# Performance work log

Hardware: AMD Instinct MI355X
Metric: run time of the kernel (lower is better)

The kernel has to match this reference:

```python
import jax, jax.numpy as jnp
import numpy as np

B, S, D = 4, 4096, 1024


def setup_inputs() -> dict:
    key = jax.random.key(0)
    ks = jax.random.split(key, 4)
    scale = 1.0 / np.sqrt(D)
    x = jax.random.normal(ks[0], (B, S, D), dtype=jnp.float32)
    Wg = jax.random.normal(ks[1], (D, D), dtype=jnp.float32) * scale
    Wv = jax.random.normal(ks[2], (D, D), dtype=jnp.float32) * scale
    Wd = jax.random.normal(ks[3], (D, D), dtype=jnp.float32) * scale
    bg = jnp.zeros((D,), dtype=jnp.float32)
    bv = jnp.zeros((D,), dtype=jnp.float32)
    bd = jnp.ones((D,), dtype=jnp.float32)  # decay_bias_init = 1.0
    return {"x": x, "Wg": Wg, "bg": bg, "Wv": Wv, "bv": bv, "Wd": Wd, "bd": bd}


def _scan_causal(x_scan, a):
    # h_t = a_t * h_{t-1} + x_t, scanned over time; x_scan, a: [B,S,D]
    def step(h, inp):
        a_t, x_t = inp
        h = a_t * h + x_t
        return h, h

    h0 = jnp.zeros(x_scan.shape[::2], dtype=x_scan.dtype)  # [B,D]
    xs = (jnp.swapaxes(a, 0, 1), jnp.swapaxes(x_scan, 0, 1))  # [S,B,D]
    _, out = jax.lax.scan(step, h0, xs)
    return jnp.swapaxes(out, 0, 1)  # back to [B,S,D]


def reference(x, Wg, bg, Wv, bv, Wd, bd):
    # nn.Linear: y = x @ W.T + b
    g = jnp.einsum('bsd,ed->bse', x, Wg) + bg
    v = jnp.einsum('bsd,ed->bse', x, Wv) + bv
    d = jnp.einsum('bsd,ed->bse', x, Wd) + bd
    x_scan = jax.nn.sigmoid(g) * jnp.tanh(v)
    a = 0.001 + 0.998 * jax.nn.sigmoid(d)
    return _scan_causal(x_scan, a)
```

## Files before the change

### kernel.cpp

```cpp
#include <hip/hip_runtime.h>
#include <cstddef>
#include <cstdint>


typedef _Float16 f16;
typedef f16 f16x4 __attribute__((ext_vector_type(4)));
typedef f16 f16x8 __attribute__((ext_vector_type(8)));
typedef float f32x4 __attribute__((ext_vector_type(4)));

#define S_LEN 4096
#define D_DIM 1024
#define B_DIM 4
#define M_TOT (B_DIM * S_LEN)
#define N_TOT (3 * D_DIM)
#define K_TOT D_DIM

#define CHUNKS 128
#define CLEN (S_LEN / CHUNKS)

__global__ void cvt_f16_kernel(const float* __restrict__ src, f16* __restrict__ dst, int n) {
  int i = (blockIdx.x * blockDim.x + threadIdx.x) * 8;
  if (i >= n) return;
  f32x4 a = *(const f32x4*)(src + i);
  f32x4 b = *(const f32x4*)(src + i + 4);
  f16x8 o;
  o[0] = (f16)a[0]; o[1] = (f16)a[1]; o[2] = (f16)a[2]; o[3] = (f16)a[3];
  o[4] = (f16)b[0]; o[5] = (f16)b[1]; o[6] = (f16)b[2]; o[7] = (f16)b[3];
  *(f16x8*)(dst + i) = o;
}

#define BM 128
#define BN 128
#define BK 32

__device__ __forceinline__ void gl_lds16(const void* g, void* l) {
  __builtin_amdgcn_global_load_lds((const __attribute__((address_space(1))) void*)g,
                                   (__attribute__((address_space(3))) void*)l, 16, 0, 0);
}

__global__ __launch_bounds__(256) void gemm_f16_kernel(const f16* __restrict__ A,
                                                       const f16* __restrict__ Bt,
                                                       f16* __restrict__ C) {
  __shared__ __attribute__((aligned(16))) f16 As[BM * BK];
  __shared__ __attribute__((aligned(16))) f16 Bs[BN * BK];
  const int tid = threadIdx.x;
  const int lane = tid & 63;
  const int wave = tid >> 6;
  const int m0 = blockIdx.y * BM;
  const int n0 = blockIdx.x * BN;

  const int srow = tid >> 2;
  const int scol = (tid & 3) * 8;
  const f16* aG0 = A + (size_t)(m0 + srow) * K_TOT + scol;
  const f16* aG1 = A + (size_t)(m0 + srow + 64) * K_TOT + scol;
  const f16* bG0 = Bt + (size_t)(n0 + srow) * K_TOT + scol;
  const f16* bG1 = Bt + (size_t)(n0 + srow + 64) * K_TOT + scol;
  f16* aL0 = &As[tid * 8];
  f16* aL1 = &As[2048 + tid * 8];
  f16* bL0 = &Bs[tid * 8];
  f16* bL1 = &Bs[2048 + tid * 8];

  const int wm = (wave >> 1) * 64;
  const int wn = (wave & 1) * 64;
  const int lm = lane & 15;
  const int kq = (lane >> 4) * 8;

  f32x4 acc[4][4] = {};

  for (int k0 = 0; k0 < K_TOT; k0 += BK) {
    gl_lds16(aG0 + k0, aL0);
    gl_lds16(aG1 + k0, aL1);
    gl_lds16(bG0 + k0, bL0);
    gl_lds16(bG1 + k0, bL1);
    __syncthreads();
    f16x8 af[4], bf[4];
#pragma unroll
    for (int i = 0; i < 4; ++i)
      af[i] = *(const f16x8*)&As[(wm + i * 16 + lm) * BK + kq];
#pragma unroll
    for (int j = 0; j < 4; ++j)
      bf[j] = *(const f16x8*)&Bs[(wn + j * 16 + lm) * BK + kq];
#pragma unroll
    for (int i = 0; i < 4; ++i)
#pragma unroll
      for (int j = 0; j < 4; ++j)
        acc[i][j] = __builtin_amdgcn_mfma_f32_16x16x32_f16(af[i], bf[j], acc[i][j], 0, 0, 0);
    __syncthreads();
  }

  const int cm = m0 + wm + (lane >> 4) * 4;
  const int cn = n0 + wn + (lane & 15);
#pragma unroll
  for (int i = 0; i < 4; ++i)
#pragma unroll
    for (int j = 0; j < 4; ++j)
#pragma unroll
      for (int r = 0; r < 4; ++r)
        C[(size_t)(cm + i * 16 + r) * N_TOT + (cn + j * 16)] = (f16)acc[i][j][r];
}

__global__ void scan1_kernel(const f16* __restrict__ G, const float* __restrict__ bg,
                             const float* __restrict__ bv, const float* __restrict__ bd,
                             f16* __restrict__ xsA, f16* __restrict__ aA,
                             float* __restrict__ P, float* __restrict__ H) {
  const int u = blockIdx.x * 256 + threadIdx.x;
  const int cg = u & 255;
  const int b = (u >> 8) & 3;
  const int ck = u >> 10;
  const int ch = cg * 4;
  const f32x4 vbg = *(const f32x4*)(bg + ch);
  const f32x4 vbv = *(const f32x4*)(bv + ch);
  const f32x4 vbd = *(const f32x4*)(bd + ch);
  f32x4 h = {0.f, 0.f, 0.f, 0.f};
  f32x4 p = {1.f, 1.f, 1.f, 1.f};
  const int t0 = ck * CLEN;
#pragma unroll 4
  for (int t = t0; t < t0 + CLEN; ++t) {
    const size_t m = (size_t)b * S_LEN + t;
    const f16* gp = G + m * N_TOT + ch;
    f16x4 g4 = *(const f16x4*)gp;
    f16x4 v4 = *(const f16x4*)(gp + D_DIM);
    f16x4 d4 = *(const f16x4*)(gp + 2 * D_DIM);
    f16x4 xs4, a4;
#pragma unroll
    for (int j = 0; j < 4; ++j) {
      float gg = (float)g4[j] + vbg[j];
      float vv = (float)v4[j] + vbv[j];
      float dd = (float)d4[j] + vbd[j];
      float sg = 1.f / (1.f + __expf(-gg));
      float tv = 1.f - 2.f / (__expf(2.f * vv) + 1.f);
      float sd = 1.f / (1.f + __expf(-dd));
      f16 xh = (f16)(sg * tv);
      f16 ah = (f16)(0.001f + 0.998f * sd);
      float xsr = (float)xh, avr = (float)ah;
      h[j] = avr * h[j] + xsr;
      p[j] *= avr;
      xs4[j] = xh;
      a4[j] = ah;
    }
    *(f16x4*)(xsA + m * D_DIM + ch) = xs4;
    *(f16x4*)(aA + m * D_DIM + ch) = a4;
  }
  const int idx = ck * 4096 + b * D_DIM + ch;
  *(f32x4*)(P + idx) = p;
  *(f32x4*)(H + idx) = h;
}

__global__ void scan2_kernel(const float* __restrict__ P, const float* __restrict__ H,
                             float* __restrict__ carry) {
  const int idx = blockIdx.x * 256 + threadIdx.x;
  float h = 0.f;
  for (int c = 0; c < CHUNKS; ++c) {
    carry[c * 4096 + idx] = h;
    h = P[c * 4096 + idx] * h + H[c * 4096 + idx];
  }
}

__global__ void scan3_kernel(const f16* __restrict__ xsA, const f16* __restrict__ aA,
                             const float* __restrict__ carry, float* __restrict__ out) {
  const int u = blockIdx.x * 256 + threadIdx.x;
  const int cg = u & 255;
  const int b = (u >> 8) & 3;
  const int ck = u >> 10;
  const int ch = cg * 4;
  f32x4 h = *(const f32x4*)(carry + ck * 4096 + b * D_DIM + ch);
  const int t0 = ck * CLEN;
#pragma unroll 4
  for (int t = t0; t < t0 + CLEN; ++t) {
    const size_t m = (size_t)b * S_LEN + t;
    f16x4 xs4 = *(const f16x4*)(xsA + m * D_DIM + ch);
    f16x4 a4 = *(const f16x4*)(aA + m * D_DIM + ch);
#pragma unroll
    for (int j = 0; j < 4; ++j) h[j] = (float)a4[j] * h[j] + (float)xs4[j];
    *(f32x4*)(out + m * D_DIM + ch) = h;
  }
}

extern "C" void kernel_launch(void* const* d_in, const int* in_sizes, int n_in,
                              void* d_out, int out_size, void* d_ws, size_t ws_size,
                              hipStream_t stream) {
  const float* x = (const float*)d_in[0];
  const float* Wg = (const float*)d_in[1];
  const float* bg = (const float*)d_in[2];
  const float* Wv = (const float*)d_in[3];
  const float* bv = (const float*)d_in[4];
  const float* Wd = (const float*)d_in[5];
  const float* bd = (const float*)d_in[6];
  float* out = (float*)d_out;

  char* ws = (char*)d_ws;
  f16* Ah = (f16*)(ws);
  f16* Bh = (f16*)(ws + 33554432);
  f16* Gh = (f16*)(ws + 39845888);
  f16* xsA = (f16*)(ws + 140509184);
  f16* aA = (f16*)(ws + 174063616);
  float* P = (float*)(ws + 207618048);
  float* H = (float*)(ws + 209715200);
  float* carry = (float*)(ws + 211812352);

  cvt_f16_kernel<<<8192, 256, 0, stream>>>(x, Ah, M_TOT * K_TOT);
  cvt_f16_kernel<<<512, 256, 0, stream>>>(Wg, Bh, D_DIM * D_DIM);
  cvt_f16_kernel<<<512, 256, 0, stream>>>(Wv, Bh + D_DIM * D_DIM, D_DIM * D_DIM);
  cvt_f16_kernel<<<512, 256, 0, stream>>>(Wd, Bh + 2 * D_DIM * D_DIM, D_DIM * D_DIM);
  gemm_f16_kernel<<<dim3(N_TOT / BN, M_TOT / BM), 256, 0, stream>>>(Ah, Bh, Gh);
  scan1_kernel<<<512, 256, 0, stream>>>(Gh, bg, bv, bd, xsA, aA, P, H);
  scan2_kernel<<<16, 256, 0, stream>>>(P, H, carry);
  scan3_kernel<<<512, 256, 0, stream>>>(xsA, aA, carry, out);
}
```

Baseline: 338.5 us.

## Fuse gate activations and chunk-local scan summary into GEMM epilogue

The GEMM now computes the g, v and d projections for one 64-column slice together, so each block holds all three matching outputs and applies the bias, sigmoid and tanh activations in its epilogue. It writes xs and a through LDS, and one wave runs a per-column scan over each 32-row chunk to emit the P and H chunk summaries. This removes the round trip of the fp16 gate tensor G and drops the separate scan1 kernel; the three weight conversions are also merged into one launch. In exchange, the serial scan runs on only 64 threads per block, the tiles are narrower, and the epilogue does more work, which may lower GEMM efficiency.

```diff
diff --git a/kernel.cpp b/kernel.cpp
--- a/kernel.cpp
+++ b/kernel.cpp
@@ -12,11 +12,13 @@
 #define D_DIM 1024
 #define B_DIM 4
 #define M_TOT (B_DIM * S_LEN)
-#define N_TOT (3 * D_DIM)
 #define K_TOT D_DIM
 
-#define CHUNKS 128
-#define CLEN (S_LEN / CHUNKS)
+#define BM 128
+#define BN 64
+#define CLEN 32
+#define CHUNKS_PER_B (S_LEN / CLEN)
+#define NCHUNK (B_DIM * CHUNKS_PER_B)
 
 __global__ void cvt_f16_kernel(const float* __restrict__ src, f16* __restrict__ dst, int n) {
   int i = (blockIdx.x * blockDim.x + threadIdx.x) * 8;
@@ -29,20 +31,34 @@
   *(f16x8*)(dst + i) = o;
 }
 
-#define BM 128
-#define BN 128
-#define BK 32
+__global__ void cvt_w_kernel(const float* __restrict__ w0, const float* __restrict__ w1,
+                             const float* __restrict__ w2, f16* __restrict__ dst) {
+  int i = (blockIdx.x * blockDim.x + threadIdx.x) * 8;
+  int sel = i >> 20;
+  int loc = i & 1048575;
+  const float* src = (sel == 0) ? w0 : (sel == 1) ? w1 : w2;
+  f32x4 a = *(const f32x4*)(src + loc);
+  f32x4 b = *(const f32x4*)(src + loc + 4);
+  f16x8 o;
+  o[0] = (f16)a[0]; o[1] = (f16)a[1]; o[2] = (f16)a[2]; o[3] = (f16)a[3];
+  o[4] = (f16)b[0]; o[5] = (f16)b[1]; o[6] = (f16)b[2]; o[7] = (f16)b[3];
+  *(f16x8*)(dst + i) = o;
+}
 
 __device__ __forceinline__ void gl_lds16(const void* g, void* l) {
   __builtin_amdgcn_global_load_lds((const __attribute__((address_space(1))) void*)g,
                                    (__attribute__((address_space(3))) void*)l, 16, 0, 0);
 }
 
-__global__ __launch_bounds__(256) void gemm_f16_kernel(const f16* __restrict__ A,
-                                                       const f16* __restrict__ Bt,
-                                                       f16* __restrict__ C) {
-  __shared__ __attribute__((aligned(16))) f16 As[BM * BK];
-  __shared__ __attribute__((aligned(16))) f16 Bs[BN * BK];
+__global__ __launch_bounds__(256) void gemm_fused_kernel(
+    const f16* __restrict__ A, const f16* __restrict__ Bh,
+    const float* __restrict__ bg, const float* __restrict__ bv, const float* __restrict__ bd,
+    f16* __restrict__ xsA, f16* __restrict__ aA,
+    float* __restrict__ P, float* __restrict__ H) {
+  __shared__ __attribute__((aligned(16))) char smem[32768];
+  f16* As = (f16*)smem;
+  f16* Bs = As + 4096;
+
   const int tid = threadIdx.x;
   const int lane = tid & 63;
   const int wave = tid >> 6;
@@ -53,106 +69,119 @@
   const int scol = (tid & 3) * 8;
   const f16* aG0 = A + (size_t)(m0 + srow) * K_TOT + scol;
   const f16* aG1 = A + (size_t)(m0 + srow + 64) * K_TOT + scol;
-  const f16* bG0 = Bt + (size_t)(n0 + srow) * K_TOT + scol;
-  const f16* bG1 = Bt + (size_t)(n0 + srow + 64) * K_TOT + scol;
-  f16* aL0 = &As[tid * 8];
-  f16* aL1 = &As[2048 + tid * 8];
-  f16* bL0 = &Bs[tid * 8];
-  f16* bL1 = &Bs[2048 + tid * 8];
+  const f16* bG0 = Bh + (size_t)(n0 + srow) * K_TOT + scol;
+  const f16* bG1 = Bh + 1048576 + (size_t)(n0 + srow) * K_TOT + scol;
+  const f16* bG2 = Bh + 2097152 + (size_t)(n0 + srow) * K_TOT + scol;
+  f16* aL0 = As + tid * 8;
+  f16* aL1 = As + 2048 + tid * 8;
+  f16* bL0 = Bs + tid * 8;
+  f16* bL1 = Bs + 2048 + tid * 8;
+  f16* bL2 = Bs + 4096 + tid * 8;
 
   const int wm = (wave >> 1) * 64;
-  const int wn = (wave & 1) * 64;
+  const int wn = (wave & 1) * 32;
   const int lm = lane & 15;
   const int kq = (lane >> 4) * 8;
 
-  f32x4 acc[4][4] = {};
-
-  for (int k0 = 0; k0 < K_TOT; k0 += BK) {
+  f32x4 acc[3][4][2] = {};
+
+  for (int k0 = 0; k0 < K_TOT; k0 += 32) {
     gl_lds16(aG0 + k0, aL0);
     gl_lds16(aG1 + k0, aL1);
     gl_lds16(bG0 + k0, bL0);
     gl_lds16(bG1 + k0, bL1);
+    gl_lds16(bG2 + k0, bL2);
     __syncthreads();
-    f16x8 af[4], bf[4];
+    f16x8 af[4];
 #pragma unroll
     for (int i = 0; i < 4; ++i)
-      af[i] = *(const f16x8*)&As[(wm + i * 16 + lm) * BK + kq];
-#pragma unroll
-    for (int j = 0; j < 4; ++j)
-      bf[j] = *(const f16x8*)&Bs[(wn + j * 16 + lm) * BK + kq];
-#pragma unroll
-    for (int i = 0; i < 4; ++i)
-#pragma unroll
-      for (int j = 0; j < 4; ++j)
-        acc[i][j] = __builtin_amdgcn_mfma_f32_16x16x32_f16(af[i], bf[j], acc[i][j], 0, 0, 0);
+      af[i] = *(const f16x8*)&As[(wm + i * 16 + lm) * 32 + kq];
+#pragma unroll
+    for (int mat = 0; mat < 3; ++mat) {
+      f16x8 bf[2];
+#pragma unroll
+      for (int j = 0; j < 2; ++j)
+        bf[j] = *(const f16x8*)&Bs[mat * 2048 + (wn + j * 16 + lm) * 32 + kq];
+#pragma unroll
+      for (int i = 0; i < 4; ++i)
+#pragma unroll
+        for (int j = 0; j < 2; ++j)
+          acc[mat][i][j] =
+              __builtin_amdgcn_mfma_f32_16x16x32_f16(af[i], bf[j], acc[mat][i][j], 0, 0, 0);
+    }
     __syncthreads();
   }
 
-  const int cm = m0 + wm + (lane >> 4) * 4;
-  const int cn = n0 + wn + (lane & 15);
+  f16* xsT = (f16*)smem;
+  f16* aT = xsT + 8192;
+
+  const int cbase = (lane >> 4) * 4;
+  float vbg[2], vbv[2], vbd[2];
+#pragma unroll
+  for (int j = 0; j < 2; ++j) {
+    int cn = n0 + wn + j * 16 + lm;
+    vbg[j] = bg[cn];
+    vbv[j] = bv[cn];
+    vbd[j] = bd[cn];
+  }
 #pragma unroll
   for (int i = 0; i < 4; ++i)
 #pragma unroll
-    for (int j = 0; j < 4; ++j)
-#pragma unroll
-      for (int r = 0; r < 4; ++r)
-        C[(size_t)(cm + i * 16 + r) * N_TOT + (cn + j * 16)] = (f16)acc[i][j][r];
-}
-
-__global__ void scan1_kernel(const f16* __restrict__ G, const float* __restrict__ bg,
-                             const float* __restrict__ bv, const float* __restrict__ bd,
-                             f16* __restrict__ xsA, f16* __restrict__ aA,
-                             float* __restrict__ P, float* __restrict__ H) {
-  const int u = blockIdx.x * 256 + threadIdx.x;
-  const int cg = u & 255;
-  const int b = (u >> 8) & 3;
-  const int ck = u >> 10;
-  const int ch = cg * 4;
-  const f32x4 vbg = *(const f32x4*)(bg + ch);
-  const f32x4 vbv = *(const f32x4*)(bv + ch);
-  const f32x4 vbd = *(const f32x4*)(bd + ch);
-  f32x4 h = {0.f, 0.f, 0.f, 0.f};
-  f32x4 p = {1.f, 1.f, 1.f, 1.f};
-  const int t0 = ck * CLEN;
-#pragma unroll 4
-  for (int t = t0; t < t0 + CLEN; ++t) {
-    const size_t m = (size_t)b * S_LEN + t;
-    const f16* gp = G + m * N_TOT + ch;
-    f16x4 g4 = *(const f16x4*)gp;
-    f16x4 v4 = *(const f16x4*)(gp + D_DIM);
-    f16x4 d4 = *(const f16x4*)(gp + 2 * D_DIM);
-    f16x4 xs4, a4;
-#pragma unroll
-    for (int j = 0; j < 4; ++j) {
-      float gg = (float)g4[j] + vbg[j];
-      float vv = (float)v4[j] + vbv[j];
-      float dd = (float)d4[j] + vbd[j];
-      float sg = 1.f / (1.f + __expf(-gg));
-      float tv = 1.f - 2.f / (__expf(2.f * vv) + 1.f);
-      float sd = 1.f / (1.f + __expf(-dd));
-      f16 xh = (f16)(sg * tv);
-      f16 ah = (f16)(0.001f + 0.998f * sd);
-      float xsr = (float)xh, avr = (float)ah;
-      h[j] = avr * h[j] + xsr;
-      p[j] *= avr;
-      xs4[j] = xh;
-      a4[j] = ah;
+    for (int j = 0; j < 2; ++j)
+#pragma unroll
+      for (int r = 0; r < 4; ++r) {
+        int rloc = wm + i * 16 + cbase + r;
+        int cloc = wn + j * 16 + lm;
+        float g = acc[0][i][j][r] + vbg[j];
+        float v = acc[1][i][j][r] + vbv[j];
+        float d = acc[2][i][j][r] + vbd[j];
+        float sg = 1.f / (1.f + __expf(-g));
+        float tv = 1.f - 2.f / (__expf(2.f * v) + 1.f);
+        float sd = 1.f / (1.f + __expf(-d));
+        xsT[rloc * 64 + cloc] = (f16)(sg * tv);
+        aT[rloc * 64 + cloc] = (f16)(0.001f + 0.998f * sd);
+      }
+  __syncthreads();
+
+  if (tid < 64) {
+    float h = 0.f, p = 1.f;
+#pragma unroll 8
+    for (int r = 0; r < 128; ++r) {
+      float av = (float)aT[r * 64 + tid];
+      float xv = (float)xsT[r * 64 + tid];
+      h = av * h + xv;
+      p *= av;
+      if ((r & 31) == 31) {
+        int sub = blockIdx.y * 4 + (r >> 5);
+        int idx = sub * D_DIM + n0 + tid;
+        P[idx] = p;
+        H[idx] = h;
+        p = 1.f;
+        h = 0.f;
+      }
     }
-    *(f16x4*)(xsA + m * D_DIM + ch) = xs4;
-    *(f16x4*)(aA + m * D_DIM + ch) = a4;
-  }
-  const int idx = ck * 4096 + b * D_DIM + ch;
-  *(f32x4*)(P + idx) = p;
-  *(f32x4*)(H + idx) = h;
+  }
+
+#pragma unroll
+  for (int it = 0; it < 4; ++it) {
+    int r = (tid >> 3) + it * 32;
+    int c = (tid & 7) * 8;
+    size_t gidx = (size_t)(m0 + r) * D_DIM + n0 + c;
+    *(f16x8*)(xsA + gidx) = *(const f16x8*)&xsT[r * 64 + c];
+    *(f16x8*)(aA + gidx) = *(const f16x8*)&aT[r * 64 + c];
+  }
 }
 
 __global__ void scan2_kernel(const float* __restrict__ P, const float* __restrict__ H,
                              float* __restrict__ carry) {
   const int idx = blockIdx.x * 256 + threadIdx.x;
+  const int b = idx >> 10;
+  const int d = idx & 1023;
   float h = 0.f;
-  for (int c = 0; c < CHUNKS; ++c) {
-    carry[c * 4096 + idx] = h;
-    h = P[c * 4096 + idx] * h + H[c * 4096 + idx];
+  for (int c = 0; c < CHUNKS_PER_B; ++c) {
+    int gs = b * CHUNKS_PER_B + c;
+    carry[gs * D_DIM + d] = h;
+    h = P[gs * D_DIM + d] * h + H[gs * D_DIM + d];
   }
 }
 
@@ -163,7 +192,8 @@
   const int b = (u >> 8) & 3;
   const int ck = u >> 10;
   const int ch = cg * 4;
-  f32x4 h = *(const f32x4*)(carry + ck * 4096 + b * D_DIM + ch);
+  const int gs = b * CHUNKS_PER_B + ck;
+  f32x4 h = *(const f32x4*)(carry + gs * D_DIM + ch);
   const int t0 = ck * CLEN;
 #pragma unroll 4
   for (int t = t0; t < t0 + CLEN; ++t) {
@@ -191,19 +221,16 @@
   char* ws = (char*)d_ws;
   f16* Ah = (f16*)(ws);
   f16* Bh = (f16*)(ws + 33554432);
-  f16* Gh = (f16*)(ws + 39845888);
-  f16* xsA = (f16*)(ws + 140509184);
-  f16* aA = (f16*)(ws + 174063616);
-  float* P = (float*)(ws + 207618048);
-  float* H = (float*)(ws + 209715200);
-  float* carry = (float*)(ws + 211812352);
+  f16* xsA = (f16*)(ws + 39845888);
+  f16* aA = (f16*)(ws + 73400320);
+  float* P = (float*)(ws + 106954752);
+  float* H = (float*)(ws + 109051904);
+  float* carry = (float*)(ws + 111149056);
 
   cvt_f16_kernel<<<8192, 256, 0, stream>>>(x, Ah, M_TOT * K_TOT);
-  cvt_f16_kernel<<<512, 256, 0, stream>>>(Wg, Bh, D_DIM * D_DIM);
-  cvt_f16_kernel<<<512, 256, 0, stream>>>(Wv, Bh + D_DIM * D_DIM, D_DIM * D_DIM);
-  cvt_f16_kernel<<<512, 256, 0, stream>>>(Wd, Bh + 2 * D_DIM * D_DIM, D_DIM * D_DIM);
-  gemm_f16_kernel<<<dim3(N_TOT / BN, M_TOT / BM), 256, 0, stream>>>(Ah, Bh, Gh);
-  scan1_kernel<<<512, 256, 0, stream>>>(Gh, bg, bv, bd, xsA, aA, P, H);
+  cvt_w_kernel<<<1536, 256, 0, stream>>>(Wg, Wv, Wd, Bh);
+  gemm_fused_kernel<<<dim3(D_DIM / BN, M_TOT / BM), 256, 0, stream>>>(
+      Ah, Bh, bg, bv, bd, xsA, aA, P, H);
   scan2_kernel<<<16, 256, 0, stream>>>(P, H, carry);
   scan3_kernel<<<512, 256, 0, stream>>>(xsA, aA, carry, out);
 }
```

New measurement: 438.6 us. 29.6% more time.
